# Performance work log

Measured on AMD Instinct MI355X. Metric: run time of the kernel, lower is better.

The kernel has to match this reference:

```python
import jax, jax.numpy as jnp
import numpy as np

B, S, D, H = 16, 1024, 768, 12
HD = D // H
SCALE = HD ** -0.5


def setup_inputs() -> dict:
    key = jax.random.key(0)
    k1, k2, k3, k4 = jax.random.split(key, 4)
    # Xavier-uniform-like init for the linear weights
    lim_qkv = (6.0 / (D + 3 * D)) ** 0.5
    lim_proj = (6.0 / (D + D)) ** 0.5
    return {
        "hidden_states": jax.random.normal(k1, (B, S, D), dtype=jnp.float32),
        "mask": jax.random.randint(k2, (B, S), 0, 2).astype(bool),
        "qkv_w": jax.random.uniform(k3, (3 * D, D), minval=-lim_qkv, maxval=lim_qkv, dtype=jnp.float32),
        "qkv_b": jnp.zeros((3 * D,), dtype=jnp.float32),
        "proj_w": jax.random.uniform(k4, (D, D), minval=-lim_proj, maxval=lim_proj, dtype=jnp.float32),
        "proj_b": jnp.zeros((D,), dtype=jnp.float32),
    }


def _masked_softmax(scores, attn_mask):
    # scores: [B,H,S,S]; attn_mask: [B,1,S,S] bool. Fully-masked rows -> all-zero
    # weights (torch gives NaN there but then zeroes the output rows; zeroing
    # the weights yields the identical final output without NaNs).
    neg_inf = jnp.finfo(scores.dtype).min
    m = jnp.max(jnp.where(attn_mask, scores, neg_inf), axis=-1, keepdims=True)
    e = jnp.where(attn_mask, jnp.exp(scores - m), 0.0)
    denom = jnp.sum(e, axis=-1, keepdims=True)
    return e / jnp.where(denom == 0, 1.0, denom)


def reference(hidden_states, mask, qkv_w, qkv_b, proj_w, proj_b):
    # fused QKV projection: [B,S,3D]
    qkv = hidden_states @ qkv_w.T + qkv_b
    qkv = qkv.reshape(B, S, 3, H, HD).transpose(2, 0, 3, 1, 4)  # [3,B,H,S,hd]
    q, k, v = qkv[0], qkv[1], qkv[2]
    tok_mask = mask[:, None, :, None]  # [B,1,S,1]
    q = jnp.where(tok_mask, q, 0.0)
    k = jnp.where(tok_mask, k, 0.0)
    v = jnp.where(tok_mask, v, 0.0)
    scores = jnp.einsum("bhqd,bhkd->bhqk", q, k) * SCALE
    attn_mask = (mask[:, :, None] & mask[:, None, :])[:, None]  # [B,1,S,S]
    attn = _masked_softmax(scores, attn_mask)
    context = jnp.einsum("bhqk,bhkd->bhqd", attn, v)
    context = context.transpose(0, 2, 1, 3).reshape(B, S, D)
    out = context @ proj_w.T + proj_b
    out = jnp.where(mask[:, :, None], out, 0.0)
    return out
```

## Files before the change

kernel.cpp:

```cpp
#include <hip/hip_runtime.h>
#include <cstdint>
#include <cstddef>

#define B 16
#define S 1024
#define D 768
#define H 12
#define HD 64
#define NTOK (B * S)
#define QKV_N (3 * D)
#define SCALE 0.125f
#define C2 2.88539008f
#define GK 768
#define NT_K 12

typedef _Float16 f16x8 __attribute__((ext_vector_type(8)));
typedef _Float16 f16x4 __attribute__((ext_vector_type(4)));
typedef __fp16 fp16x2 __attribute__((ext_vector_type(2)));
typedef float f32x4 __attribute__((ext_vector_type(4)));
typedef int i32x4 __attribute__((ext_vector_type(4)));

typedef __attribute__((address_space(3))) void as3_void;
typedef const __attribute__((address_space(1))) void as1_void;

#if defined(__has_builtin)
#if __has_builtin(__builtin_amdgcn_exp2f)
#define EXP2(x) __builtin_amdgcn_exp2f(x)
#else
#define EXP2(x) exp2f(x)
#endif
#else
#define EXP2(x) exp2f(x)
#endif

#define BARRIER() asm volatile("s_barrier" ::: "memory")

union PPack { f16x8 h; i32x4 i; };
union CPack { fp16x2 h; int i; };

__global__ __launch_bounds__(256) void normalize_mask_kernel(
    const unsigned char* __restrict__ raw, int* __restrict__ outm, int n) {
    __shared__ int s_isbyte;
    const int tid = threadIdx.x;
    if (tid == 0) s_isbyte = 0;
    __syncthreads();
    int found = 0;
    for (int i = tid; i < n; i += 256) {
        if ((i & 3) != 0 && raw[i] != 0) found = 1;
    }
    if (found) atomicOr(&s_isbyte, 1);
    __syncthreads();
    const int isbyte = s_isbyte;
    if (isbyte) {
        for (int i = tid; i < n; i += 256) outm[i] = raw[i] ? 1 : 0;
    } else {
        const int* r32 = (const int*)raw;
        for (int i = tid; i < n; i += 256) outm[i] = r32[i] ? 1 : 0;
    }
}

__global__ __launch_bounds__(256) void cvt_all_f16(
    const float* __restrict__ in0, _Float16* __restrict__ out0, int n0,
    const float* __restrict__ in1, _Float16* __restrict__ out1, int n1,
    const float* __restrict__ in2, _Float16* __restrict__ out2, int n2) {
    int i = blockIdx.x * 256 + threadIdx.x;
    const float* in;
    _Float16* out;
    if (i < n0) { in = in0; out = out0; }
    else if (i < n0 + n1) { i -= n0; in = in1; out = out1; }
    else { i -= n0 + n1; in = in2; out = out2; if (i >= n2) return; }
    const float4 v = ((const float4*)in)[i];
    f16x4 o;
    o[0] = (_Float16)v.x; o[1] = (_Float16)v.y;
    o[2] = (_Float16)v.z; o[3] = (_Float16)v.w;
    ((f16x4*)out)[i] = o;
}

template <int MODE>
__global__ __launch_bounds__(256, 2) void gemm16(
    const _Float16* __restrict__ A, const _Float16* __restrict__ Wm,
    const float* __restrict__ bias, const int* __restrict__ rowmask,
    int N, float* __restrict__ outf, _Float16* __restrict__ outh,
    _Float16* __restrict__ vtb) {
    __shared__ _Float16 smem[32768];

    const int tid = threadIdx.x;
    const int w = tid >> 6, l = tid & 63;
    const int wm = (w >> 1) * 64, wn = (w & 1) * 64;
    const int lg = l >> 4, lc = l & 15;

    const int bid = blockIdx.x;
    const int xcd = bid & 7;
    const int idx = bid >> 3;
    const int bn = (idx >> 4) * 128;
    const int bm = (xcd * 16 + (idx & 15)) * 128;

    f32x4 acc[4][4] = {};

#define STAGE(T, BUF)                                                           \
    {                                                                           \
        const int kt_ = (T) * 64;                                               \
        _Pragma("unroll")                                                       \
        for (int i_ = 0; i_ < 4; ++i_) {                                        \
            const int ci_ = (w << 2) + i_;                           \
            const int r_ = (ci_ << 3) + (l >> 3);                               \
            const int c16_ = (l & 7) ^ (r_ & 7);                                \
            __builtin_amdgcn_global_load_lds(                                   \
                (as1_void*)(A + (size_t)(bm + r_) * GK + kt_ + c16_ * 8),       \
                (as3_void*)(smem + (BUF) * 8192 + ci_ * 512), 16, 0, 0);        \
            __builtin_amdgcn_global_load_lds(                                   \
                (as1_void*)(Wm + (size_t)(bn + r_) * GK + kt_ + c16_ * 8),      \
                (as3_void*)(smem + 16384 + (BUF) * 8192 + ci_ * 512), 16, 0, 0);\
        }                                                                       \
    }

    STAGE(0, 0)

    for (int t = 0; t < NT_K; ++t) {
        const int cur = t & 1;
        if (t + 1 < NT_K) {
            STAGE(t + 1, cur ^ 1)
            asm volatile("s_waitcnt vmcnt(8)" ::: "memory");
        } else {
            asm volatile("s_waitcnt vmcnt(0)" ::: "memory");
        }
        BARRIER();

        const _Float16* sA = smem + cur * 8192;
        const _Float16* sB = smem + 16384 + cur * 8192;
        __builtin_amdgcn_s_setprio(1);
#pragma unroll
        for (int kk = 0; kk < 2; ++kk) {
            const int c16 = ((kk << 2) + lg) ^ (lc & 7);
            f16x8 af[4], bf[4];
#pragma unroll
            for (int ni = 0; ni < 4; ++ni)
                bf[ni] = *(const f16x8*)&sB[(wn + ni * 16 + lc) * 64 + c16 * 8];
#pragma unroll
            for (int mi = 0; mi < 4; ++mi)
                af[mi] = *(const f16x8*)&sA[(wm + mi * 16 + lc) * 64 + c16 * 8];
#pragma unroll
            for (int mi = 0; mi < 4; ++mi)
#pragma unroll
                for (int ni = 0; ni < 4; ++ni)
                    acc[mi][ni] = __builtin_amdgcn_mfma_f32_16x16x32_f16(
                        af[mi], bf[ni], acc[mi][ni], 0, 0, 0);
        }
        __builtin_amdgcn_s_setprio(0);
        BARRIER();
    }
#undef STAGE

    float bs[4];
#pragma unroll
    for (int ni = 0; ni < 4; ++ni) bs[ni] = bias[bn + wn + ni * 16 + lc];

    if (MODE == 1) {
        if (bn < 1536) {
#pragma unroll
            for (int mi = 0; mi < 4; ++mi) {
#pragma unroll
                for (int j = 0; j < 4; ++j) {
                    const int m = bm + wm + mi * 16 + lg * 4 + j;
#pragma unroll
                    for (int ni = 0; ni < 4; ++ni) {
                        const int col = bn + wn + ni * 16 + lc;
                        outh[(size_t)m * N + col] =
                            (_Float16)(acc[mi][ni][j] + bs[ni]);
                    }
                }
            }
        } else {
#pragma unroll
            for (int mi = 0; mi < 4; ++mi) {
#pragma unroll
                for (int ni = 0; ni < 4; ++ni) {
                    f16x4 v4;
#pragma unroll
                    for (int j = 0; j < 4; ++j)
                        v4[j] = (_Float16)(acc[mi][ni][j] + bs[ni]);
                    const int nl = wn + ni * 16 + lc;
                    const int ml = wm + mi * 16 + lg * 4;
                    *(f16x4*)&smem[nl * 136 + ml] = v4;
                }
            }
            __syncthreads();
            const int r = tid >> 1;
            const int c0 = (tid & 1) * 64;
            const int col0 = bn - 1536 + r;
            const int hh = col0 >> 6, hd = col0 & 63;
            const int bb = bm >> 10;
            const int s0 = (bm & 1023) + c0;
            _Float16* dst = vtb + ((size_t)(bb * H + hh) * HD + hd) * S + s0;
#pragma unroll
            for (int e = 0; e < 8; ++e)
                *(f16x8*)(dst + e * 8) = *(const f16x8*)&smem[r * 136 + c0 + e * 8];
        }
    } else {
#pragma unroll
        for (int mi = 0; mi < 4; ++mi) {
#pragma unroll
            for (int j = 0; j < 4; ++j) {
                const int m = bm + wm + mi * 16 + lg * 4 + j;
                const int mv = rowmask[m];
#pragma unroll
                for (int ni = 0; ni < 4; ++ni) {
                    const int col = bn + wn + ni * 16 + lc;
                    outf[(size_t)m * N + col] = mv ? acc[mi][ni][j] + bs[ni] : 0.f;
                }
            }
        }
    }
}

__global__ __launch_bounds__(256, 3) void attn_kernel(
    const _Float16* __restrict__ qkv, const _Float16* __restrict__ vtb,
    const int* __restrict__ mask, _Float16* __restrict__ ctx) {
    __shared__ _Float16 ksm[3][64 * 64];
    __shared__ _Float16 vsm[3][64 * 64];
    __shared__ float mbias[S];

    const int blk = blockIdx.x;
    const int xcd = blk & 7;
    const int idx = blk >> 3;
    const int bh_ = xcd * 24 + (idx >> 2);
    const int qt = idx & 3;
    const int h = bh_ % H;
    const int b = bh_ / H;
    const int tid = threadIdx.x;
    const int w = tid >> 6, lane = tid & 63;
    const int lg = lane >> 4, lc = lane & 15;

    const size_t bh = (size_t)(b * H + h);
    const _Float16* Kp = qkv + (size_t)(b * S) * QKV_N + D + h * HD;
    const _Float16* Vt = vtb + bh * HD * S;
    const int* mrow = mask + b * S;

    const int r0 = w * 8 + (lane >> 3);
    const int swz8 = ((lane & 7) ^ (r0 & 7)) * 8;
    const int koff0 = r0 * QKV_N + swz8;
    const int koff1 = (32 + r0) * QKV_N + swz8;
    const int voff0 = r0 * S + swz8;
    const int voff1 = (32 + r0) * S + swz8;

#define STAGE(T, BUF)                                                          \
    {                                                                          \
        const int kt_ = (T) * 64;                                              \
        __builtin_amdgcn_global_load_lds(                                      \
            (as1_void*)(Kp + (size_t)kt_ * QKV_N + koff0),                     \
            (as3_void*)(&ksm[BUF][w * 512]), 16, 0, 0);                        \
        __builtin_amdgcn_global_load_lds(                                      \
            (as1_void*)(Kp + (size_t)kt_ * QKV_N + koff1),                     \
            (as3_void*)(&ksm[BUF][2048 + w * 512]), 16, 0, 0);                 \
        __builtin_amdgcn_global_load_lds(                                      \
            (as1_void*)(Vt + (size_t)kt_ + voff0),                            \
            (as3_void*)(&vsm[BUF][w * 512]), 16, 0, 0);                        \
        __builtin_amdgcn_global_load_lds(                                      \
            (as1_void*)(Vt + (size_t)kt_ + voff1),                            \
            (as3_void*)(&vsm[BUF][2048 + w * 512]), 16, 0, 0);                 \
    }

    const int qbase = qt * 256 + w * 16 + lc;
    const _Float16 qs = (_Float16)(0.125f * 1.44269504f);
    f16x8 qf[4][2];
#pragma unroll
    for (int qg = 0; qg < 4; ++qg) {
        const _Float16* Qp =
            qkv + (size_t)(b * S + qbase + qg * 64) * QKV_N + h * HD;
        qf[qg][0] = *(const f16x8*)(Qp + lg * 8);
        qf[qg][1] = *(const f16x8*)(Qp + 32 + lg * 8);
        qf[qg][0] *= qs;
        qf[qg][1] *= qs;
    }

#pragma unroll
    for (int i = 0; i < 4; ++i)
        mbias[i * 256 + tid] = mrow[i * 256 + tid] ? -C2 : -1e9f;

    STAGE(0, 0)
    STAGE(1, 1)

    f32x4 acc[4][4] = {};
    float lsum[4] = {0.f, 0.f, 0.f, 0.f};
    fp16x2 ones;
    ones[0] = (__fp16)1.0f; ones[1] = (__fp16)1.0f;

    int cur = 0;
    for (int it = 0; it < S / 64; ++it) {
        if (it == 0)
            asm volatile("s_waitcnt vmcnt(4) lgkmcnt(0)" ::: "memory");
        else if (it < S / 64 - 1)
            asm volatile("s_waitcnt vmcnt(4)" ::: "memory");
        else
            asm volatile("s_waitcnt vmcnt(0)" ::: "memory");
        BARRIER();

        if (it + 2 < S / 64) {
            int nb = cur + 2; if (nb >= 3) nb -= 3;
            STAGE(it + 2, nb)
        }

        __builtin_amdgcn_s_setprio(1);
#pragma unroll
        for (int u = 0; u < 2; ++u) {
            PPack pp8[4];
#pragma unroll
            for (int s = 0; s < 2; ++s) {
                const int t = 2 * u + s;
                const int krow = (t * 16 + lc) * 64;
                const f16x8 kfa =
                    *(const f16x8*)&ksm[cur][krow + (lg ^ (lc & 7)) * 8];
                const f16x8 kfb =
                    *(const f16x8*)&ksm[cur][krow + ((4 + lg) ^ (lc & 7)) * 8];
                const f32x4 mb = *(const f32x4*)&mbias[it * 64 + t * 16 + 4 * lg];
#pragma unroll
                for (int qg = 0; qg < 4; ++qg) {
                    f32x4 c = mb;
                    c = __builtin_amdgcn_mfma_f32_16x16x32_f16(kfa, qf[qg][0], c, 0, 0, 0);
                    c = __builtin_amdgcn_mfma_f32_16x16x32_f16(kfb, qf[qg][1], c, 0, 0, 0);
                    CPack u0, u1;
                    u0.h = __builtin_amdgcn_cvt_pkrtz(EXP2(c[0]), EXP2(c[1]));
                    u1.h = __builtin_amdgcn_cvt_pkrtz(EXP2(c[2]), EXP2(c[3]));
                    lsum[qg] = __builtin_amdgcn_fdot2(u0.h, ones, lsum[qg], false);
                    lsum[qg] = __builtin_amdgcn_fdot2(u1.h, ones, lsum[qg], false);
                    pp8[qg].i[s * 2 + 0] = u0.i;
                    pp8[qg].i[s * 2 + 1] = u1.i;
                }
            }

#pragma unroll
            for (int g = 0; g < 4; ++g) {
                const int vrow = (g * 16 + lc) * 64;
                const int cA = ((4 * u + (lg >> 1)) ^ (lc & 7)) * 8 + (lg & 1) * 4;
                const int cB = ((4 * u + 2 + (lg >> 1)) ^ (lc & 7)) * 8 + (lg & 1) * 4;
                const f16x4 vlo = *(const f16x4*)&vsm[cur][vrow + cA];
                const f16x4 vhi = *(const f16x4*)&vsm[cur][vrow + cB];
                f16x8 vf8;
                vf8[0] = vlo[0]; vf8[1] = vlo[1]; vf8[2] = vlo[2]; vf8[3] = vlo[3];
                vf8[4] = vhi[0]; vf8[5] = vhi[1]; vf8[6] = vhi[2]; vf8[7] = vhi[3];
#pragma unroll
                for (int qg = 0; qg < 4; ++qg)
                    acc[qg][g] = __builtin_amdgcn_mfma_f32_16x16x32_f16(
                        pp8[qg].h, vf8, acc[qg][g], 0, 0, 0);
            }
        }
        __builtin_amdgcn_s_setprio(0);
        if (++cur >= 3) cur = 0;
    }
#undef STAGE

#pragma unroll
    for (int qg = 0; qg < 4; ++qg) {
        float l = lsum[qg];
        l += __shfl_xor(l, 16);
        l += __shfl_xor(l, 32);
        const float inv = l > 0.f ? 1.f / l : 0.f;
#pragma unroll
        for (int j = 0; j < 4; ++j) {
            const int qin = 4 * lg + j;
            const float ij = __shfl(inv, qin);
            const int qr = qt * 256 + qg * 64 + w * 16 + qin;
            const float iq = mrow[qr] ? ij : 0.f;
            const size_t o = ((size_t)(b * S + qr)) * D + h * HD;
#pragma unroll
            for (int g = 0; g < 4; ++g)
                ctx[o + 16 * g + lc] = (_Float16)(acc[qg][g][j] * iq);
        }
    }
}

extern "C" void kernel_launch(void* const* d_in, const int* in_sizes, int n_in,
                              void* d_out, int out_size, void* d_ws, size_t ws_size,
                              hipStream_t stream) {
    const float* hidden = (const float*)d_in[0];
    const unsigned char* maskraw = (const unsigned char*)d_in[1];
    const float* qkv_w = (const float*)d_in[2];
    const float* qkv_b = (const float*)d_in[3];
    const float* proj_w = (const float*)d_in[4];
    const float* proj_b = (const float*)d_in[5];
    float* out = (float*)d_out;

    char* ws = (char*)d_ws;
    size_t off = 0;
    int* maskN = (int*)(ws + off);            off += (size_t)NTOK * 4;
    _Float16* hid16 = (_Float16*)(ws + off);  off += (size_t)NTOK * D * 2;
    _Float16* qkvw16 = (_Float16*)(ws + off); off += (size_t)QKV_N * D * 2;
    _Float16* projw16 = (_Float16*)(ws + off); off += (size_t)D * D * 2;
    _Float16* qkv16 = (_Float16*)(ws + off);  off += (size_t)NTOK * QKV_N * 2;
    _Float16* vt = (_Float16*)(ws + off);     off += (size_t)NTOK * D * 2;
    _Float16* ctx16 = (_Float16*)(ws + off);  off += (size_t)NTOK * D * 2;

    normalize_mask_kernel<<<1, 256, 0, stream>>>(maskraw, maskN, NTOK);

    const int n0 = NTOK * D / 4, n1 = QKV_N * D / 4, n2 = D * D / 4;
    cvt_all_f16<<<(n0 + n1 + n2 + 255) / 256, 256, 0, stream>>>(
        hidden, hid16, n0, qkv_w, qkvw16, n1, proj_w, projw16, n2);

    gemm16<1><<<dim3(2304), 256, 0, stream>>>(
        hid16, qkvw16, qkv_b, nullptr, QKV_N, nullptr, qkv16, vt);

    attn_kernel<<<dim3(B * H * (S / 256)), 256, 0, stream>>>(qkv16, vt, maskN, ctx16);

    gemm16<0><<<dim3(768), 256, 0, stream>>>(
        ctx16, projw16, proj_b, maskN, D, out, nullptr, nullptr);
}
```

Measured before the change: 191.2 us.

## Widen GEMM tile to 128x256 with triple-buffered BK=32 pipeline and fuse prep kernels

Result: faster. 176.6 us (-7.6%).

```diff
diff --git a/kernel.cpp b/kernel.cpp
--- a/kernel.cpp
+++ b/kernel.cpp
@@ -12,7 +12,7 @@
 #define SCALE 0.125f
 #define C2 2.88539008f
 #define GK 768
-#define NT_K 12
+#define NT32 24
 
 typedef _Float16 f16x8 __attribute__((ext_vector_type(8)));
 typedef _Float16 f16x4 __attribute__((ext_vector_type(4)));
@@ -38,32 +38,25 @@
 union PPack { f16x8 h; i32x4 i; };
 union CPack { fp16x2 h; int i; };
 
-__global__ __launch_bounds__(256) void normalize_mask_kernel(
-    const unsigned char* __restrict__ raw, int* __restrict__ outm, int n) {
-    __shared__ int s_isbyte;
-    const int tid = threadIdx.x;
-    if (tid == 0) s_isbyte = 0;
-    __syncthreads();
-    int found = 0;
-    for (int i = tid; i < n; i += 256) {
-        if ((i & 3) != 0 && raw[i] != 0) found = 1;
-    }
-    if (found) atomicOr(&s_isbyte, 1);
-    __syncthreads();
-    const int isbyte = s_isbyte;
-    if (isbyte) {
-        for (int i = tid; i < n; i += 256) outm[i] = raw[i] ? 1 : 0;
-    } else {
-        const int* r32 = (const int*)raw;
-        for (int i = tid; i < n; i += 256) outm[i] = r32[i] ? 1 : 0;
-    }
-}
-
-__global__ __launch_bounds__(256) void cvt_all_f16(
+__global__ __launch_bounds__(256) void prep_kernel(
+    const unsigned char* __restrict__ raw, int* __restrict__ outm,
     const float* __restrict__ in0, _Float16* __restrict__ out0, int n0,
     const float* __restrict__ in1, _Float16* __restrict__ out1, int n1,
     const float* __restrict__ in2, _Float16* __restrict__ out2, int n2) {
-    int i = blockIdx.x * 256 + threadIdx.x;
+    const int bid = blockIdx.x;
+    const int tid = threadIdx.x;
+    if (bid < 64) {
+        __shared__ int s_isbyte;
+        if (tid == 0) s_isbyte = 0;
+        __syncthreads();
+        const int gi = bid * 256 + tid;
+        if ((gi & 3) != 0 && raw[gi] != 0) atomicOr(&s_isbyte, 1);
+        __syncthreads();
+        if (s_isbyte) outm[gi] = raw[gi] ? 1 : 0;
+        else outm[gi] = ((const int*)raw)[gi] ? 1 : 0;
+        return;
+    }
+    int i = (bid - 64) * 256 + tid;
     const float* in;
     _Float16* out;
     if (i < n0) { in = in0; out = out0; }
@@ -77,83 +70,90 @@
 }
 
 template <int MODE>
-__global__ __launch_bounds__(256, 2) void gemm16(
+__global__ __launch_bounds__(256, 2) void gemm_bt(
     const _Float16* __restrict__ A, const _Float16* __restrict__ Wm,
     const float* __restrict__ bias, const int* __restrict__ rowmask,
-    int N, float* __restrict__ outf, _Float16* __restrict__ outh,
+    float* __restrict__ outf, _Float16* __restrict__ outh,
     _Float16* __restrict__ vtb) {
-    __shared__ _Float16 smem[32768];
+    __shared__ _Float16 smem[36864];
 
     const int tid = threadIdx.x;
     const int w = tid >> 6, l = tid & 63;
-    const int wm = (w >> 1) * 64, wn = (w & 1) * 64;
+    const int wm = (w >> 1) * 64, wn = (w & 1) * 128;
     const int lg = l >> 4, lc = l & 15;
 
     const int bid = blockIdx.x;
     const int xcd = bid & 7;
     const int idx = bid >> 3;
-    const int bn = (idx >> 4) * 128;
+    const int bn = (idx >> 4) * 256;
     const int bm = (xcd * 16 + (idx & 15)) * 128;
 
-    f32x4 acc[4][4] = {};
-
-#define STAGE(T, BUF)                                                           \
-    {                                                                           \
-        const int kt_ = (T) * 64;                                               \
-        _Pragma("unroll")                                                       \
-        for (int i_ = 0; i_ < 4; ++i_) {                                        \
-            const int ci_ = (w << 2) + i_;                           \
-            const int r_ = (ci_ << 3) + (l >> 3);                               \
-            const int c16_ = (l & 7) ^ (r_ & 7);                                \
-            __builtin_amdgcn_global_load_lds(                                   \
-                (as1_void*)(A + (size_t)(bm + r_) * GK + kt_ + c16_ * 8),       \
-                (as3_void*)(smem + (BUF) * 8192 + ci_ * 512), 16, 0, 0);        \
-            __builtin_amdgcn_global_load_lds(                                   \
-                (as1_void*)(Wm + (size_t)(bn + r_) * GK + kt_ + c16_ * 8),      \
-                (as3_void*)(smem + 16384 + (BUF) * 8192 + ci_ * 512), 16, 0, 0);\
-        }                                                                       \
-    }
-
-    STAGE(0, 0)
-
-    for (int t = 0; t < NT_K; ++t) {
-        const int cur = t & 1;
-        if (t + 1 < NT_K) {
-            STAGE(t + 1, cur ^ 1)
-            asm volatile("s_waitcnt vmcnt(8)" ::: "memory");
-        } else {
+    const int lrow = l >> 2;
+    const int sw8h = ((l & 3) ^ ((l >> 3) & 3)) * 8;
+
+    f32x4 acc[4][8] = {};
+
+#define STG(T, BUF)                                                            \
+    {                                                                          \
+        const int kt_ = (T) * 32;                                              \
+        _Pragma("unroll")                                                      \
+        for (int i_ = 0; i_ < 2; ++i_) {                                       \
+            const int cA_ = i_ * 4 + w;                              \
+            __builtin_amdgcn_global_load_lds(                                  \
+                (as1_void*)(A + (size_t)(bm + cA_ * 16 + lrow) * GK + kt_ + sw8h), \
+                (as3_void*)(smem + (BUF) * 12288 + cA_ * 512), 16, 0, 0);      \
+        }                                                                      \
+        _Pragma("unroll")                                                      \
+        for (int i_ = 0; i_ < 4; ++i_) {                                       \
+            const int cB_ = i_ * 4 + w;                             \
+            __builtin_amdgcn_global_load_lds(                                  \
+                (as1_void*)(Wm + (size_t)(bn + cB_ * 16 + lrow) * GK + kt_ + sw8h), \
+                (as3_void*)(smem + (BUF) * 12288 + 4096 + cB_ * 512), 16, 0, 0); \
+        }                                                                      \
+    }
+
+    STG(0, 0)
+    STG(1, 1)
+
+    const int c16h = (lg ^ ((lc >> 1) & 3)) * 8;
+    int cur = 0;
+    for (int t = 0; t < NT32; ++t) {
+        if (t < NT32 - 1)
+            asm volatile("s_waitcnt vmcnt(6)" ::: "memory");
+        else
             asm volatile("s_waitcnt vmcnt(0)" ::: "memory");
-        }
         BARRIER();
 
-        const _Float16* sA = smem + cur * 8192;
-        const _Float16* sB = smem + 16384 + cur * 8192;
+        if (t + 2 < NT32) {
+            int nb = cur + 2; if (nb >= 3) nb -= 3;
+            STG(t + 2, nb)
+        }
+
+        const _Float16* sA = smem + cur * 12288;
+        const _Float16* sB = sA + 4096;
+        f16x8 af[4], bf[8];
+#pragma unroll
+        for (int mi = 0; mi < 4; ++mi)
+            af[mi] = *(const f16x8*)&sA[(wm + mi * 16 + lc) * 32 + c16h];
+#pragma unroll
+        for (int ni = 0; ni < 8; ++ni)
+            bf[ni] = *(const f16x8*)&sB[(wn + ni * 16 + lc) * 32 + c16h];
+
         __builtin_amdgcn_s_setprio(1);
 #pragma unroll
-        for (int kk = 0; kk < 2; ++kk) {
-            const int c16 = ((kk << 2) + lg) ^ (lc & 7);
-            f16x8 af[4], bf[4];
-#pragma unroll
-            for (int ni = 0; ni < 4; ++ni)
-                bf[ni] = *(const f16x8*)&sB[(wn + ni * 16 + lc) * 64 + c16 * 8];
-#pragma unroll
-            for (int mi = 0; mi < 4; ++mi)
-                af[mi] = *(const f16x8*)&sA[(wm + mi * 16 + lc) * 64 + c16 * 8];
-#pragma unroll
-            for (int mi = 0; mi < 4; ++mi)
-#pragma unroll
-                for (int ni = 0; ni < 4; ++ni)
-                    acc[mi][ni] = __builtin_amdgcn_mfma_f32_16x16x32_f16(
-                        af[mi], bf[ni], acc[mi][ni], 0, 0, 0);
-        }
+        for (int mi = 0; mi < 4; ++mi)
+#pragma unroll
+            for (int ni = 0; ni < 8; ++ni)
+                acc[mi][ni] = __builtin_amdgcn_mfma_f32_16x16x32_f16(
+                    af[mi], bf[ni], acc[mi][ni], 0, 0, 0);
         __builtin_amdgcn_s_setprio(0);
-        BARRIER();
-    }
-#undef STAGE
-
-    float bs[4];
-#pragma unroll
-    for (int ni = 0; ni < 4; ++ni) bs[ni] = bias[bn + wn + ni * 16 + lc];
+        if (++cur >= 3) cur = 0;
+    }
+#undef STG
+
+    float bs[8];
+#pragma unroll
+    for (int ni = 0; ni < 8; ++ni) bs[ni] = bias[bn + wn + ni * 16 + lc];
 
     if (MODE == 1) {
         if (bn < 1536) {
@@ -163,18 +163,19 @@
                 for (int j = 0; j < 4; ++j) {
                     const int m = bm + wm + mi * 16 + lg * 4 + j;
 #pragma unroll
-                    for (int ni = 0; ni < 4; ++ni) {
+                    for (int ni = 0; ni < 8; ++ni) {
                         const int col = bn + wn + ni * 16 + lc;
-                        outh[(size_t)m * N + col] =
+                        outh[(size_t)m * QKV_N + col] =
                             (_Float16)(acc[mi][ni][j] + bs[ni]);
                     }
                 }
             }
         } else {
+            BARRIER();
 #pragma unroll
             for (int mi = 0; mi < 4; ++mi) {
 #pragma unroll
-                for (int ni = 0; ni < 4; ++ni) {
+                for (int ni = 0; ni < 8; ++ni) {
                     f16x4 v4;
 #pragma unroll
                     for (int j = 0; j < 4; ++j)
@@ -184,17 +185,15 @@
                     *(f16x4*)&smem[nl * 136 + ml] = v4;
                 }
             }
-            __syncthreads();
-            const int r = tid >> 1;
-            const int c0 = (tid & 1) * 64;
-            const int col0 = bn - 1536 + r;
+            BARRIER();
+            const int col0 = bn - 1536 + tid;
             const int hh = col0 >> 6, hd = col0 & 63;
             const int bb = bm >> 10;
-            const int s0 = (bm & 1023) + c0;
+            const int s0 = bm & 1023;
             _Float16* dst = vtb + ((size_t)(bb * H + hh) * HD + hd) * S + s0;
 #pragma unroll
-            for (int e = 0; e < 8; ++e)
-                *(f16x8*)(dst + e * 8) = *(const f16x8*)&smem[r * 136 + c0 + e * 8];
+            for (int e = 0; e < 16; ++e)
+                *(f16x8*)(dst + e * 8) = *(const f16x8*)&smem[tid * 136 + e * 8];
         }
     } else {
 #pragma unroll
@@ -204,9 +203,9 @@
                 const int m = bm + wm + mi * 16 + lg * 4 + j;
                 const int mv = rowmask[m];
 #pragma unroll
-                for (int ni = 0; ni < 4; ++ni) {
+                for (int ni = 0; ni < 8; ++ni) {
                     const int col = bn + wn + ni * 16 + lc;
-                    outf[(size_t)m * N + col] = mv ? acc[mi][ni][j] + bs[ni] : 0.f;
+                    outf[(size_t)m * D + col] = mv ? acc[mi][ni][j] + bs[ni] : 0.f;
                 }
             }
         }
@@ -390,17 +389,15 @@
     _Float16* vt = (_Float16*)(ws + off);     off += (size_t)NTOK * D * 2;
     _Float16* ctx16 = (_Float16*)(ws + off);  off += (size_t)NTOK * D * 2;
 
-    normalize_mask_kernel<<<1, 256, 0, stream>>>(maskraw, maskN, NTOK);
-
     const int n0 = NTOK * D / 4, n1 = QKV_N * D / 4, n2 = D * D / 4;
-    cvt_all_f16<<<(n0 + n1 + n2 + 255) / 256, 256, 0, stream>>>(
-        hidden, hid16, n0, qkv_w, qkvw16, n1, proj_w, projw16, n2);
-
-    gemm16<1><<<dim3(2304), 256, 0, stream>>>(
-        hid16, qkvw16, qkv_b, nullptr, QKV_N, nullptr, qkv16, vt);
+    prep_kernel<<<dim3(64 + (n0 + n1 + n2 + 255) / 256), 256, 0, stream>>>(
+        maskraw, maskN, hidden, hid16, n0, qkv_w, qkvw16, n1, proj_w, projw16, n2);
+
+    gemm_bt<1><<<dim3(1152), 256, 0, stream>>>(
+        hid16, qkvw16, qkv_b, nullptr, nullptr, qkv16, vt);
 
     attn_kernel<<<dim3(B * H * (S / 256)), 256, 0, stream>>>(qkv16, vt, maskN, ctx16);
 
-    gemm16<0><<<dim3(768), 256, 0, stream>>>(
-        ctx16, projw16, proj_b, maskN, D, out, nullptr, nullptr);
+    gemm_bt<0><<<dim3(384), 256, 0, stream>>>(
+        ctx16, projw16, proj_b, maskN, out, nullptr, nullptr);
 }
```
